# Kernel tuning notes

Measured on AMD Instinct MI355X. Metric: run time of the kernel, lower is better.

Reference implementation:

```python
import jax, jax.numpy as jnp
import numpy as np
import math

D_MODEL = 128      # embedding_dim
D_STATE = 64
D_CONV = 4
NHEADS = 4         # d_inner / headdim (Mamba2 default headdim=64)
HEADDIM = 64
D_INNER = 256      # expand * d_model
CONV_DIM = 384     # d_inner + 2*ngroups*d_state (ngroups=1)
D_IN_PROJ = 644    # 2*d_inner + 2*ngroups*d_state + nheads
NLAYERS = 2
INPUT_DIM = 768
EPS = 1e-5


def setup_inputs() -> dict:
    key = jax.random.key(0)
    ks = jax.random.split(key, 20)
    rn = lambda k, s, sd=0.02: jax.random.normal(k, s, jnp.float32) * sd
    return {
        "x": jax.random.normal(ks[0], (16, 1024, INPUT_DIM), jnp.float32),
        "fc1_W": rn(ks[1], (INPUT_DIM, D_MODEL)),
        "fc1_b": jnp.zeros((D_MODEL,), jnp.float32),
        "ln_w": jnp.ones((NLAYERS, D_MODEL), jnp.float32),
        "ln_b": jnp.zeros((NLAYERS, D_MODEL), jnp.float32),
        "in_W": rn(ks[2], (NLAYERS, D_MODEL, D_IN_PROJ)),
        "conv_w": rn(ks[3], (NLAYERS, D_CONV, CONV_DIM), 0.1),
        "conv_b": jnp.zeros((NLAYERS, CONV_DIM), jnp.float32),
        "dt_bias": rn(ks[4], (NLAYERS, NHEADS), 0.5),
        "A_log": jnp.log(jax.random.uniform(ks[5], (NLAYERS, NHEADS), jnp.float32, 1.0, 16.0)),
        "Dp": jnp.ones((NLAYERS, NHEADS), jnp.float32),
        "rms_w": jnp.ones((NLAYERS, D_INNER), jnp.float32),
        "out_W": rn(ks[6], (NLAYERS, D_INNER, D_MODEL)),
        "fc2_W1": rn(ks[7], (D_MODEL, D_MODEL)),
        "fc2_b1": jnp.zeros((D_MODEL,), jnp.float32),
        "fc2_W2": rn(ks[8], (D_MODEL, 6)),
        "fc2_b2": jnp.zeros((6,), jnp.float32),
    }


def _pos_embedding(L):
    pos = jnp.arange(L, dtype=jnp.float32)[:, None]                       # (L,1)
    div = jnp.exp(jnp.arange(0, D_MODEL, 2, dtype=jnp.float32) * (-math.log(10000.0) / D_MODEL))
    pe = jnp.zeros((L, D_MODEL), jnp.float32)
    pe = pe.at[:, 0::2].set(jnp.sin(pos * div))
    pe = pe.at[:, 1::2].set(jnp.cos(pos * div))
    return pe[None]                                                        # (1,L,D)


def _layernorm(x, w, b):
    mu = jnp.mean(x, -1, keepdims=True)
    var = jnp.mean(jnp.square(x - mu), -1, keepdims=True)
    return (x - mu) * jax.lax.rsqrt(var + EPS) * w + b


def _mamba2(u, in_W, conv_w, conv_b, dt_bias, A_log, Dp, rms_w, out_W):
    b, l, _ = u.shape
    zxbcdt = u @ in_W                                                      # (b,l,644)
    z = zxbcdt[..., :D_INNER]
    xBC = zxbcdt[..., D_INNER:D_INNER + CONV_DIM]
    dt = jax.nn.softplus(zxbcdt[..., D_INNER + CONV_DIM:] + dt_bias)       # (b,l,h)
    # causal depthwise conv1d (width 4) + SiLU
    xp = jnp.pad(xBC, ((0, 0), (D_CONV - 1, 0), (0, 0)))
    xc = conv_b
    for k in range(D_CONV):
        xc = xc + conv_w[k] * xp[:, k:k + l, :]
    xc = jax.nn.silu(xc)                                                   # (b,l,384)
    xh = xc[..., :D_INNER].reshape(b, l, NHEADS, HEADDIM)                  # (b,l,h,p)
    B = xc[..., D_INNER:D_INNER + D_STATE]                                 # (b,l,n)
    C = xc[..., D_INNER + D_STATE:]                                        # (b,l,n)
    A = -jnp.exp(A_log)                                                    # (h,)
    dA = jnp.exp(dt * A)                                                   # (b,l,h)
    dtx = dt[..., None] * xh                                               # (b,l,h,p)

    def step(h, inp):
        dA_t, dtx_t, B_t, C_t = inp                                        # (b,h),(b,h,p),(b,n),(b,n)
        h = dA_t[..., None, None] * h + dtx_t[..., None] * B_t[:, None, None, :]
        y = jnp.einsum('bhpn,bn->bhp', h, C_t)
        return h, y

    h0 = jnp.zeros((b, NHEADS, HEADDIM, D_STATE), u.dtype)
    _, ys = jax.lax.scan(step, h0, (dA.transpose(1, 0, 2), dtx.transpose(1, 0, 2, 3),
                                    B.transpose(1, 0, 2), C.transpose(1, 0, 2)))
    y = ys.transpose(1, 0, 2, 3) + Dp[None, None, :, None] * xh            # (b,l,h,p)
    y = y.reshape(b, l, D_INNER)
    # gated RMSNorm: rmsnorm(y * silu(z)) * weight
    y = y * jax.nn.silu(z)
    y = y * jax.lax.rsqrt(jnp.mean(jnp.square(y), -1, keepdims=True) + EPS) * rms_w
    return y @ out_W


def reference(x, fc1_W, fc1_b, ln_w, ln_b, in_W, conv_w, conv_b, dt_bias,
              A_log, Dp, rms_w, out_W, fc2_W1, fc2_b1, fc2_W2, fc2_b2):
    h = x @ fc1_W + fc1_b                                                  # (b,l,128)
    h = h + _pos_embedding(h.shape[1])
    for i in range(NLAYERS):
        res = h
        hn = _layernorm(h, ln_w[i], ln_b[i])
        h = _mamba2(hn, in_W[i], conv_w[i], conv_b[i], dt_bias[i],
                    A_log[i], Dp[i], rms_w[i], out_W[i]) + res
        # dropout: identity in eval mode
    h = jax.nn.leaky_relu(h @ fc2_W1 + fc2_b1, negative_slope=0.1)
    return h @ fc2_W2 + fc2_b2                                             # (b,l,6)
```

## Files before the change

### kernel.cpp

```cpp
#include <hip/hip_runtime.h>
#include <hip/hip_bf16.h>

#define BATCH 16
#define SEQ 1024
#define NROWS (BATCH*SEQ)
#define IN_DIM 768
#define DM 128
#define DIP 644
#define DI 256
#define CDIM 384
#define DST 64
#define NH 4
#define HD 64
#define CHUNK 64
#define NCHUNK (SEQ/CHUNK)

#define WB_FC1   0
#define WB_IN    98304
#define WB_OUT   263168
#define WB_FC2   328704
#define WB_TOTAL 345088

typedef __attribute__((ext_vector_type(8))) short short8;
typedef __attribute__((ext_vector_type(4))) float float4v;

__device__ __forceinline__ short f2b(float f) {
    unsigned u = __builtin_bit_cast(unsigned, f);
    u += 0x7fffu + ((u >> 16) & 1u);
    return (short)(u >> 16);
}
__device__ __forceinline__ float s2f(short s) {
    unsigned u = ((unsigned)(unsigned short)s) << 16;
    return __builtin_bit_cast(float, u);
}
__device__ __forceinline__ float silu(float a) { return a / (1.f + expf(-a)); }

__global__ void prep_weights(const float* __restrict__ fc1_W, const float* __restrict__ in_W,
                             const float* __restrict__ out_W, const float* __restrict__ fc2_W1,
                             short* __restrict__ wb) {
    int idx = blockIdx.x * 256 + threadIdx.x;
    if (idx < 98304) {
        int n = idx / 768, k = idx % 768;
        wb[WB_FC1 + idx] = f2b(fc1_W[k * 128 + n]);
        return;
    }
    idx -= 98304;
    if (idx < 2 * 82432) {
        int l = idx / 82432, r = idx % 82432;
        int n = r / 128, k = r % 128;
        wb[WB_IN + idx] = f2b(in_W[(size_t)l * 82432 + k * 644 + n]);
        return;
    }
    idx -= 164864;
    if (idx < 2 * 32768) {
        int l = idx / 32768, r = idx % 32768;
        int n = r / 256, k = r % 256;
        wb[WB_OUT + idx] = f2b(out_W[(size_t)l * 32768 + k * 128 + n]);
        return;
    }
    idx -= 65536;
    if (idx < 16384) {
        int n = idx / 128, k = idx % 128;
        wb[WB_FC2 + idx] = f2b(fc2_W1[k * 128 + n]);
    }
}

#define GEMM_PROLOGUE() \
    int tid = threadIdx.x; \
    int lane = tid & 63; \
    int m = lane & 15; \
    int kq = (lane >> 4) * 8; \
    int w = tid >> 6; \
    int mrow = (w & 3) * 16; \
    int ngrp = w >> 2; \
    int a_off = (mrow + m) * 72 + kq; \
    int b_off = (ngrp * 64 + m) * 72 + kq; \
    int ar = tid >> 3; \
    int ak = (tid & 7) * 8; \
    (void)ar; (void)ak; \
    float4v acc[4]; \
    acc[0] = (float4v)0.f; acc[1] = (float4v)0.f; acc[2] = (float4v)0.f; acc[3] = (float4v)0.f;

#define GEMM_COMPUTE_TILE() \
    { \
        short8 a0 = *reinterpret_cast<const short8*>(&As[a_off]); \
        short8 a1 = *reinterpret_cast<const short8*>(&As[a_off + 32]); \
        _Pragma("unroll") \
        for (int nt = 0; nt < 4; nt++) { \
            short8 b0 = *reinterpret_cast<const short8*>(&Bt[b_off + nt * 16 * 72]); \
            short8 b1 = *reinterpret_cast<const short8*>(&Bt[b_off + nt * 16 * 72 + 32]); \
            acc[nt] = __builtin_amdgcn_mfma_f32_16x16x32_bf16(a0, b0, acc[nt], 0, 0, 0); \
            acc[nt] = __builtin_amdgcn_mfma_f32_16x16x32_bf16(a1, b1, acc[nt], 0, 0, 0); \
        } \
    }

#define GEMM_STAGE_B(wtptr, LDB, k0) \
    _Pragma("unroll") \
    for (int i = 0; i < 2; i++) { \
        int idx = tid + i * 512; \
        int n = idx >> 3, kk = (idx & 7) * 8; \
        *reinterpret_cast<short8*>(&Bt[n * 72 + kk]) = \
            *reinterpret_cast<const short8*>(&wtptr[n * (LDB) + (k0) + kk]); \
    }

__global__ __launch_bounds__(512) void fc1_mfma(const float* __restrict__ x,
                                                const short* __restrict__ wt,
                                                const float* __restrict__ bias,
                                                const float* __restrict__ lnw0,
                                                const float* __restrict__ lnb0,
                                                float* __restrict__ h,
                                                short* __restrict__ hnb) {
    __shared__ short As[32 * 72];
    __shared__ short Bt[128 * 72];
    __shared__ float ps1[32][4], ps2[32][4];
    int tid = threadIdx.x;
    int lane = tid & 63;
    int m = lane & 15;
    int quad = lane >> 4;
    int kq = quad * 8;
    int w = tid >> 6;
    int mrow = (w & 1) * 16;
    int ngrp = w >> 1;
    int ar = tid >> 4;
    int ac = (tid & 15) * 4;
    int row0 = blockIdx.x * 32;
    float4v acc[2];
    acc[0] = (float4v)0.f; acc[1] = (float4v)0.f;
    for (int kt = 0; kt < 12; kt++) {
        int k0 = kt * 64;
        if (kt) __syncthreads();
        {
            const float* src = x + (size_t)(row0 + ar) * IN_DIM + k0 + ac;
            float4 v = *(const float4*)src;
            short4 pv;
            pv.x = f2b(v.x); pv.y = f2b(v.y); pv.z = f2b(v.z); pv.w = f2b(v.w);
            *reinterpret_cast<short4*>(&As[ar * 72 + ac]) = pv;
        }
        GEMM_STAGE_B(wt, 768, k0);
        __syncthreads();
        short8 a0 = *reinterpret_cast<const short8*>(&As[(mrow + m) * 72 + kq]);
        short8 a1 = *reinterpret_cast<const short8*>(&As[(mrow + m) * 72 + kq + 32]);
        #pragma unroll
        for (int nt = 0; nt < 2; nt++) {
            int bo = (ngrp * 32 + nt * 16 + m) * 72 + kq;
            short8 b0 = *reinterpret_cast<const short8*>(&Bt[bo]);
            short8 b1 = *reinterpret_cast<const short8*>(&Bt[bo + 32]);
            acc[nt] = __builtin_amdgcn_mfma_f32_16x16x32_bf16(a0, b0, acc[nt], 0, 0, 0);
            acc[nt] = __builtin_amdgcn_mfma_f32_16x16x32_bf16(a1, b1, acc[nt], 0, 0, 0);
        }
    }
    float val[2][4];
    float s1r[4] = {0.f,0.f,0.f,0.f}, s2r[4] = {0.f,0.f,0.f,0.f};
    #pragma unroll
    for (int nt = 0; nt < 2; nt++) {
        int col = ngrp * 32 + nt * 16 + m;
        float bv = bias[col];
        float div = expf(-(float)(col & ~1) * 0.071955784f);
        #pragma unroll
        for (int r = 0; r < 4; r++) {
            int row = row0 + mrow + quad * 4 + r;
            int t = row & (SEQ - 1);
            float arg = (float)t * div;
            float pe = (col & 1) ? cosf(arg) : sinf(arg);
            float v = acc[nt][r] + bv + pe;
            val[nt][r] = v;
            s1r[r] += v; s2r[r] += v * v;
        }
    }
    #pragma unroll
    for (int o = 1; o < 16; o <<= 1) {
        #pragma unroll
        for (int r = 0; r < 4; r++) {
            s1r[r] += __shfl_xor(s1r[r], o);
            s2r[r] += __shfl_xor(s2r[r], o);
        }
    }
    if (m == 0) {
        #pragma unroll
        for (int r = 0; r < 4; r++) {
            ps1[mrow + quad * 4 + r][ngrp] = s1r[r];
            ps2[mrow + quad * 4 + r][ngrp] = s2r[r];
        }
    }
    __syncthreads();
    #pragma unroll
    for (int r = 0; r < 4; r++) {
        int rl = mrow + quad * 4 + r;
        float s1 = ps1[rl][0] + ps1[rl][1] + ps1[rl][2] + ps1[rl][3];
        float s2 = ps2[rl][0] + ps2[rl][1] + ps2[rl][2] + ps2[rl][3];
        float mu = s1 * (1.f / 128.f);
        float rs = rsqrtf(s2 * (1.f / 128.f) - mu * mu + 1e-5f);
        int row = row0 + rl;
        #pragma unroll
        for (int nt = 0; nt < 2; nt++) {
            int col = ngrp * 32 + nt * 16 + m;
            float v = val[nt][r];
            h[(size_t)row * DM + col] = v;
            hnb[(size_t)row * DM + col] = f2b((v - mu) * rs * lnw0[col] + lnb0[col]);
        }
    }
}

__global__ __launch_bounds__(512) void inproj_mfma(const short* __restrict__ hnb,
                                                   const short* __restrict__ wb,
                                                   short* __restrict__ zb,
                                                   short* __restrict__ xbc,
                                                   int layer) {
    __shared__ short As[64 * 72];
    __shared__ short Bt[128 * 72];
    GEMM_PROLOGUE();
    int row0 = blockIdx.x * 64;
    int ncol0 = blockIdx.y * 128;
    const short* wt = wb + WB_IN + (size_t)layer * 82432;
    for (int kt = 0; kt < 2; kt++) {
        int k0 = kt * 64;
        if (kt) __syncthreads();
        *reinterpret_cast<short8*>(&As[ar * 72 + ak]) =
            *reinterpret_cast<const short8*>(&hnb[(size_t)(row0 + ar) * DM + k0 + ak]);
        #pragma unroll
        for (int i = 0; i < 2; i++) {
            int idx = tid + i * 512;
            int n = idx >> 3, kk = (idx & 7) * 8;
            *reinterpret_cast<short8*>(&Bt[n * 72 + kk]) =
                *reinterpret_cast<const short8*>(&wt[(ncol0 + n) * 128 + k0 + kk]);
        }
        __syncthreads();
        GEMM_COMPUTE_TILE();
    }
    int colbase = ncol0 + ngrp * 64;
    if (ncol0 < DI) {
        #pragma unroll
        for (int nt = 0; nt < 4; nt++) {
            int col = colbase + nt * 16 + m;
            #pragma unroll
            for (int r = 0; r < 4; r++) {
                int row = row0 + mrow + (lane >> 4) * 4 + r;
                zb[(size_t)row * DI + col] = f2b(acc[nt][r]);
            }
        }
    } else {
        int xbase = colbase - DI;
        #pragma unroll
        for (int nt = 0; nt < 4; nt++) {
            int col = xbase + nt * 16 + m;
            #pragma unroll
            for (int r = 0; r < 4; r++) {
                int row = row0 + mrow + (lane >> 4) * 4 + r;
                xbc[(size_t)row * CDIM + col] = f2b(acc[nt][r]);
            }
        }
    }
}

__global__ void conv_kernel(const short* __restrict__ xbc,
                            const float* __restrict__ convw, const float* __restrict__ convb,
                            short* __restrict__ xcb,
                            const short* __restrict__ hnb, const short* __restrict__ wb,
                            const float* __restrict__ dt_bias, float* __restrict__ dtb,
                            int layer) {
    int c = threadIdx.x;
    int row0 = blockIdx.x * 4;
    int l0 = row0 & (SEQ - 1);
    const float* cw = convw + (size_t)layer * 4 * CDIM;
    float w0 = cw[c], w1 = cw[CDIM + c], w2 = cw[2 * CDIM + c], w3 = cw[3 * CDIM + c];
    float bb = convb[layer * CDIM + c];
    float v[7];
    #pragma unroll
    for (int i = 0; i < 7; i++) {
        int rr = row0 + i - 3;
        v[i] = (l0 + i - 3 >= 0) ? s2f(xbc[(size_t)rr * CDIM + c]) : 0.f;
    }
    #pragma unroll
    for (int j = 0; j < 4; j++) {
        float acc = bb + w0 * v[j] + w1 * v[j + 1] + w2 * v[j + 2] + w3 * v[j + 3];
        xcb[(size_t)(row0 + j) * CDIM + c] = f2b(silu(acc));
    }
    if (c < 128) {
        int r = c >> 5;
        int rem = c & 31;
        int hh = rem >> 3;
        int part = rem & 7;
        const short* hrow = hnb + (size_t)(row0 + r) * DM + part * 16;
        const short* wrow = wb + WB_IN + (size_t)layer * 82432 + (640 + hh) * 128 + part * 16;
        short8 hv0 = *reinterpret_cast<const short8*>(hrow);
        short8 hv1 = *reinterpret_cast<const short8*>(hrow + 8);
        short8 wv0 = *reinterpret_cast<const short8*>(wrow);
        short8 wv1 = *reinterpret_cast<const short8*>(wrow + 8);
        float s = 0.f;
        #pragma unroll
        for (int q = 0; q < 8; q++)
            s += s2f(hv0[q]) * s2f(wv0[q]) + s2f(hv1[q]) * s2f(wv1[q]);
        s += __shfl_xor(s, 1);
        s += __shfl_xor(s, 2);
        s += __shfl_xor(s, 4);
        if (part == 0) {
            float raw = s + dt_bias[layer * NH + hh];
            float dt = (raw > 20.f) ? raw : log1pf(expf(raw));
            dtb[(size_t)(row0 + r) * NH + hh] = dt;
        }
    }
}

__global__ __launch_bounds__(256) void chunk_state_mfma(const short* __restrict__ xcb,
                                                        const float* __restrict__ dtb,
                                                        const float* __restrict__ A_log,
                                                        short* __restrict__ Slocb,
                                                        float* __restrict__ decay, int layer) {
    __shared__ short XTw[64 * 72];
    __shared__ short BT[64 * 72];
    __shared__ float wst[64];
    int bid = blockIdx.x;
    int c  = bid & (NCHUNK - 1);
    int hh = (bid >> 4) & (NH - 1);
    int b  = bid >> 6;
    int tid = threadIdx.x;
    int row0 = b * SEQ + c * CHUNK;
    float A = -expf(A_log[layer * NH + hh]);

    if (tid < CHUNK) {
        float dtv = dtb[(size_t)(row0 + tid) * NH + hh];
        float l = dtv * A;
        #pragma unroll
        for (int o = 1; o < 64; o <<= 1) { float v = __shfl_up(l, o); if (tid >= o) l += v; }
        float Ltot = __shfl(l, 63);
        wst[tid] = expf(Ltot - l) * dtv;
        if (tid == 63) decay[bid] = expf(Ltot);
    }
    __syncthreads();
    {
        int p = tid & 63;
        int tb0 = tid >> 6;
        #pragma unroll
        for (int i = 0; i < 2; i++) {
            int t0 = (tb0 + i * 4) * 8;
            short8 xv, bv;
            #pragma unroll
            for (int j = 0; j < 8; j++) {
                int t = t0 + j;
                const short* xr = xcb + (size_t)(row0 + t) * CDIM;
                xv[j] = f2b(s2f(xr[hh * HD + p]) * wst[t]);
                bv[j] = xr[DI + p];
            }
            *reinterpret_cast<short8*>(&XTw[p * 72 + t0]) = xv;
            *reinterpret_cast<short8*>(&BT[p * 72 + t0]) = bv;
        }
    }
    __syncthreads();

    int lane = tid & 63;
    int m = lane & 15;
    int kq = (lane >> 4) * 8;
    int w = tid >> 6;
    int a_off = (w * 16 + m) * 72 + kq;
    float4v acc[4];
    acc[0] = (float4v)0.f; acc[1] = (float4v)0.f; acc[2] = (float4v)0.f; acc[3] = (float4v)0.f;
    short8 a0 = *reinterpret_cast<const short8*>(&XTw[a_off]);
    short8 a1 = *reinterpret_cast<const short8*>(&XTw[a_off + 32]);
    #pragma unroll
    for (int nt = 0; nt < 4; nt++) {
        int bo = (nt * 16 + m) * 72 + kq;
        short8 b0 = *reinterpret_cast<const short8*>(&BT[bo]);
        short8 b1 = *reinterpret_cast<const short8*>(&BT[bo + 32]);
        acc[nt] = __builtin_amdgcn_mfma_f32_16x16x32_bf16(a0, b0, acc[nt], 0, 0, 0);
        acc[nt] = __builtin_amdgcn_mfma_f32_16x16x32_bf16(a1, b1, acc[nt], 0, 0, 0);
    }
    short* Sp = Slocb + (size_t)bid * (HD * DST);
    int tq = (lane >> 4) * 4;
    #pragma unroll
    for (int nt = 0; nt < 4; nt++) {
        #pragma unroll
        for (int r = 0; r < 4; r++) {
            int p = w * 16 + tq + r;
            int n = nt * 16 + m;
            Sp[p * DST + n] = f2b(acc[nt][r]);
        }
    }
}

__global__ __launch_bounds__(256) void chunk_out_mfma(const short* __restrict__ xcb,
                                                      const float* __restrict__ dtb,
                                                      const float* __restrict__ A_log,
                                                      const float* __restrict__ Dpw,
                                                      const short* __restrict__ Slocb,
                                                      const float* __restrict__ decay,
                                                      short* __restrict__ ybb, int layer) {
    __shared__ short Cb[64 * 72];
    __shared__ short Bb[64 * 72];
    __shared__ short XT[64 * 72];
    __shared__ short HT[64 * 72];
    __shared__ float Ls[64], dts[64];
    int bid = blockIdx.x;
    int c  = bid & (NCHUNK - 1);
    int hh = (bid >> 4) & (NH - 1);
    int b  = bid >> 6;
    int tid = threadIdx.x;
    int row0 = b * SEQ + c * CHUNK;
    int bh0 = bid & ~(NCHUNK - 1);
    float A = -expf(A_log[layer * NH + hh]);
    float Dph = Dpw[layer * NH + hh];

    if (tid < CHUNK) {
        float dtv = dtb[(size_t)(row0 + tid) * NH + hh];
        float l = dtv * A;
        #pragma unroll
        for (int o = 1; o < 64; o <<= 1) { float v = __shfl_up(l, o); if (tid >= o) l += v; }
        Ls[tid] = l;
        dts[tid] = dtv;
    }
    {
        float hreg[16];
        #pragma unroll
        for (int k = 0; k < 16; k++) hreg[k] = 0.f;
        for (int j = 0; j < c; j++) {
            float d = decay[bh0 + j];
            const short* Sp = Slocb + (size_t)(bh0 + j) * (HD * DST) + tid * 16;
            short8 s0 = *reinterpret_cast<const short8*>(Sp);
            short8 s1 = *reinterpret_cast<const short8*>(Sp + 8);
            #pragma unroll
            for (int k = 0; k < 8; k++) {
                hreg[k]     = d * hreg[k]     + s2f(s0[k]);
                hreg[8 + k] = d * hreg[8 + k] + s2f(s1[k]);
            }
        }
        int p = tid >> 2;
        int n0 = (tid & 3) * 16;
        short8 h0, h1;
        #pragma unroll
        for (int k = 0; k < 8; k++) { h0[k] = f2b(hreg[k]); h1[k] = f2b(hreg[8 + k]); }
        *reinterpret_cast<short8*>(&HT[p * 72 + n0]) = h0;
        *reinterpret_cast<short8*>(&HT[p * 72 + n0 + 8]) = h1;
    }
    {
        int p = tid & 63;
        int tb0 = tid >> 6;
        #pragma unroll
        for (int i = 0; i < 2; i++) {
            int t0 = (tb0 + i * 4) * 8;
            short8 xv;
            #pragma unroll
            for (int j = 0; j < 8; j++)
                xv[j] = xcb[(size_t)(row0 + t0 + j) * CDIM + hh * HD + p];
            *reinterpret_cast<short8*>(&XT[p * 72 + t0]) = xv;
        }
    }
    #pragma unroll
    for (int i = 0; i < 2; i++) {
        int idx = tid + i * 256;
        int t = idx >> 3, cb = (idx & 7) * 8;
        const short* xr = xcb + (size_t)(row0 + t) * CDIM;
        *reinterpret_cast<short8*>(&Bb[t * 72 + cb]) =
            *reinterpret_cast<const short8*>(&xr[DI + cb]);
        *reinterpret_cast<short8*>(&Cb[t * 72 + cb]) =
            *reinterpret_cast<const short8*>(&xr[DI + DST + cb]);
    }
    __syncthreads();

    int lane = tid & 63;
    int m = lane & 15;
    int kq = (lane >> 4) * 8;
    int w = tid >> 6;
    int tq = (lane >> 4) * 4;
    int a_off = (w * 16 + m) * 72 + kq;

    short8 ca0 = *reinterpret_cast<const short8*>(&Cb[a_off]);
    short8 ca1 = *reinterpret_cast<const short8*>(&Cb[a_off + 32]);

    float4v g[4], ir[4];
    #pragma unroll
    for (int i = 0; i < 4; i++) { g[i] = (float4v)0.f; ir[i] = (float4v)0.f; }
    #pragma unroll
    for (int st = 0; st < 4; st++) {
        int bo = (st * 16 + m) * 72 + kq;
        short8 b0 = *reinterpret_cast<const short8*>(&Bb[bo]);
        short8 b1 = *reinterpret_cast<const short8*>(&Bb[bo + 32]);
        g[st] = __builtin_amdgcn_mfma_f32_16x16x32_bf16(ca0, b0, g[st], 0, 0, 0);
        g[st] = __builtin_amdgcn_mfma_f32_16x16x32_bf16(ca1, b1, g[st], 0, 0, 0);
        short8 h0 = *reinterpret_cast<const short8*>(&HT[bo]);
        short8 h1 = *reinterpret_cast<const short8*>(&HT[bo + 32]);
        ir[st] = __builtin_amdgcn_mfma_f32_16x16x32_bf16(ca0, h0, ir[st], 0, 0, 0);
        ir[st] = __builtin_amdgcn_mfma_f32_16x16x32_bf16(ca1, h1, ir[st], 0, 0, 0);
    }
    __syncthreads();
    #pragma unroll
    for (int st = 0; st < 4; st++) {
        #pragma unroll
        for (int r = 0; r < 4; r++) {
            int t = w * 16 + tq + r;
            int s = st * 16 + m;
            float mv = 0.f;
            if (s <= t) mv = g[st][r] * expf(Ls[t] - Ls[s]) * dts[s];
            Bb[t * 72 + s] = f2b(mv);
        }
    }
    __syncthreads();
    float4v yi[4];
    #pragma unroll
    for (int i = 0; i < 4; i++) yi[i] = (float4v)0.f;
    short8 ma0 = *reinterpret_cast<const short8*>(&Bb[a_off]);
    short8 ma1 = *reinterpret_cast<const short8*>(&Bb[a_off + 32]);
    #pragma unroll
    for (int pt = 0; pt < 4; pt++) {
        int bo = (pt * 16 + m) * 72 + kq;
        short8 x0 = *reinterpret_cast<const short8*>(&XT[bo]);
        short8 x1 = *reinterpret_cast<const short8*>(&XT[bo + 32]);
        yi[pt] = __builtin_amdgcn_mfma_f32_16x16x32_bf16(ma0, x0, yi[pt], 0, 0, 0);
        yi[pt] = __builtin_amdgcn_mfma_f32_16x16x32_bf16(ma1, x1, yi[pt], 0, 0, 0);
    }
    #pragma unroll
    for (int r = 0; r < 4; r++) {
        int t = w * 16 + tq + r;
        float et = expf(Ls[t]);
        short* yr = ybb + (size_t)(row0 + t) * DI + hh * HD;
        #pragma unroll
        for (int pt = 0; pt < 4; pt++) {
            int p = pt * 16 + m;
            float xv = s2f(XT[p * 72 + t]);
            yr[p] = f2b(yi[pt][r] + et * ir[pt][r] + Dph * xv);
        }
    }
}

__global__ __launch_bounds__(512) void outproj_gate_mfma(const short* __restrict__ ybb,
                                                         const short* __restrict__ zb,
                                                         const float* __restrict__ rmsw,
                                                         const short* __restrict__ wb,
                                                         const float* __restrict__ lnw2,
                                                         const float* __restrict__ lnb2,
                                                         float* __restrict__ h,
                                                         short* __restrict__ hnb,
                                                         const float* __restrict__ fc2_b1,
                                                         const float* __restrict__ fc2_W2,
                                                         const float* __restrict__ fc2_b2,
                                                         float* __restrict__ outp,
                                                         int layer, int do_fc2) {
    __shared__ __align__(16) char smem[36864];
    short* As = (short*)smem;
    short* Bt = (short*)(smem + 9216);
    float* hs = (float*)smem;
    short* As2 = (short*)smem;
    short* Bt2 = (short*)(smem + 17408);
    float* h2s = (float*)smem;
    __shared__ float rs_s[64];
    __shared__ float w2s[768];
    GEMM_PROLOGUE();
    int row0 = blockIdx.x * 64;
    const short* wt = wb + WB_OUT + (size_t)layer * 32768;
    if (do_fc2)
        for (int i = tid; i < 768; i += 512) w2s[i] = fc2_W2[i];
    {
        int r = tid >> 3, j = tid & 7;
        const short8* yr = (const short8*)(ybb + (size_t)(row0 + r) * DI + j * 32);
        const short8* zr = (const short8*)(zb + (size_t)(row0 + r) * DI + j * 32);
        float s2 = 0.f;
        #pragma unroll
        for (int i = 0; i < 4; i++) {
            short8 yv = yr[i];
            short8 zv = zr[i];
            #pragma unroll
            for (int q = 0; q < 8; q++) {
                float v = s2f(yv[q]) * silu(s2f(zv[q]));
                s2 += v * v;
            }
        }
        #pragma unroll
        for (int o = 1; o < 8; o <<= 1) s2 += __shfl_xor(s2, o);
        if (j == 0) rs_s[r] = rsqrtf(s2 * (1.f / 256.f) + 1e-5f);
    }
    __syncthreads();
    for (int kt = 0; kt < 4; kt++) {
        int k0 = kt * 64;
        if (kt) __syncthreads();
        {
            int k = k0 + ak;
            short8 yv = *(const short8*)(ybb + (size_t)(row0 + ar) * DI + k);
            short8 zv = *(const short8*)(zb + (size_t)(row0 + ar) * DI + k);
            float4 w0 = *(const float4*)(rmsw + layer * DI + k);
            float4 w1 = *(const float4*)(rmsw + layer * DI + k + 4);
            float rs = rs_s[ar];
            short8 av;
            av[0] = f2b(s2f(yv[0]) * silu(s2f(zv[0])) * rs * w0.x);
            av[1] = f2b(s2f(yv[1]) * silu(s2f(zv[1])) * rs * w0.y);
            av[2] = f2b(s2f(yv[2]) * silu(s2f(zv[2])) * rs * w0.z);
            av[3] = f2b(s2f(yv[3]) * silu(s2f(zv[3])) * rs * w0.w);
            av[4] = f2b(s2f(yv[4]) * silu(s2f(zv[4])) * rs * w1.x);
            av[5] = f2b(s2f(yv[5]) * silu(s2f(zv[5])) * rs * w1.y);
            av[6] = f2b(s2f(yv[6]) * silu(s2f(zv[6])) * rs * w1.z);
            av[7] = f2b(s2f(yv[7]) * silu(s2f(zv[7])) * rs * w1.w);
            *reinterpret_cast<short8*>(&As[ar * 72 + ak]) = av;
        }
        GEMM_STAGE_B(wt, 256, k0);
        __syncthreads();
        GEMM_COMPUTE_TILE();
    }
    __syncthreads();
    #pragma unroll
    for (int nt = 0; nt < 4; nt++) {
        int col = ngrp * 64 + nt * 16 + m;
        #pragma unroll
        for (int r = 0; r < 4; r++) {
            int rr = mrow + (lane >> 4) * 4 + r;
            hs[rr * 133 + col] = acc[nt][r];
        }
    }
    __syncthreads();
    int er = tid >> 3, ej = tid & 7;
    int erow = row0 + er;
    float vals[16];
    {
        const float* hsrc = h + (size_t)erow * DM + ej * 16;
        float s1 = 0.f, s2 = 0.f;
        #pragma unroll
        for (int i = 0; i < 4; i++) {
            float4 ho = *(const float4*)(hsrc + i * 4);
            float v0 = ho.x + hs[er * 133 + ej * 16 + i * 4];
            float v1 = ho.y + hs[er * 133 + ej * 16 + i * 4 + 1];
            float v2 = ho.z + hs[er * 133 + ej * 16 + i * 4 + 2];
            float v3 = ho.w + hs[er * 133 + ej * 16 + i * 4 + 3];
            vals[i*4] = v0; vals[i*4+1] = v1; vals[i*4+2] = v2; vals[i*4+3] = v3;
            s1 += v0 + v1 + v2 + v3;
            s2 += v0*v0 + v1*v1 + v2*v2 + v3*v3;
        }
        if (!do_fc2) {
            #pragma unroll
            for (int o = 1; o < 8; o <<= 1) { s1 += __shfl_xor(s1, o); s2 += __shfl_xor(s2, o); }
            float* hdst = h + (size_t)erow * DM + ej * 16;
            #pragma unroll
            for (int i = 0; i < 4; i++)
                *(float4*)(hdst + i * 4) = make_float4(vals[i*4], vals[i*4+1], vals[i*4+2], vals[i*4+3]);
            float mu = s1 * (1.f / 128.f);
            float rs = rsqrtf(s2 * (1.f / 128.f) - mu * mu + 1e-5f);
            const float* lw = lnw2 + ej * 16;
            const float* lb = lnb2 + ej * 16;
            short8 a0, a1;
            #pragma unroll
            for (int i = 0; i < 8; i++) {
                a0[i] = f2b((vals[i] - mu) * rs * lw[i] + lb[i]);
                a1[i] = f2b((vals[8 + i] - mu) * rs * lw[8 + i] + lb[8 + i]);
            }
            short* hndst = hnb + (size_t)erow * DM + ej * 16;
            *reinterpret_cast<short8*>(hndst) = a0;
            *reinterpret_cast<short8*>(hndst + 8) = a1;
        }
    }
    if (!do_fc2) return;

    __syncthreads();
    {
        short8 a0p, a1p;
        #pragma unroll
        for (int i = 0; i < 8; i++) { a0p[i] = f2b(vals[i]); a1p[i] = f2b(vals[8 + i]); }
        *reinterpret_cast<short8*>(&As2[er * 136 + ej * 16]) = a0p;
        *reinterpret_cast<short8*>(&As2[er * 136 + ej * 16 + 8]) = a1p;
    }
    const short* wtf = wb + WB_FC2;
    float4v acc2[4];
    acc2[0] = (float4v)0.f; acc2[1] = (float4v)0.f; acc2[2] = (float4v)0.f; acc2[3] = (float4v)0.f;
    for (int kt = 0; kt < 2; kt++) {
        int k0 = kt * 64;
        __syncthreads();
        #pragma unroll
        for (int i = 0; i < 2; i++) {
            int idx = tid + i * 512;
            int n = idx >> 3, kk = (idx & 7) * 8;
            *reinterpret_cast<short8*>(&Bt2[n * 72 + kk]) =
                *reinterpret_cast<const short8*>(&wtf[n * 128 + k0 + kk]);
        }
        __syncthreads();
        short8 a0 = *reinterpret_cast<const short8*>(&As2[(mrow + m) * 136 + k0 + kq]);
        short8 a1 = *reinterpret_cast<const short8*>(&As2[(mrow + m) * 136 + k0 + kq + 32]);
        #pragma unroll
        for (int nt = 0; nt < 4; nt++) {
            int bo = (ngrp * 64 + nt * 16 + m) * 72 + kq;
            short8 b0 = *reinterpret_cast<const short8*>(&Bt2[bo]);
            short8 b1 = *reinterpret_cast<const short8*>(&Bt2[bo + 32]);
            acc2[nt] = __builtin_amdgcn_mfma_f32_16x16x32_bf16(a0, b0, acc2[nt], 0, 0, 0);
            acc2[nt] = __builtin_amdgcn_mfma_f32_16x16x32_bf16(a1, b1, acc2[nt], 0, 0, 0);
        }
    }
    __syncthreads();
    #pragma unroll
    for (int nt = 0; nt < 4; nt++) {
        int col = ngrp * 64 + nt * 16 + m;
        float bv = fc2_b1[col];
        #pragma unroll
        for (int r = 0; r < 4; r++) {
            int rr = mrow + (lane >> 4) * 4 + r;
            float o = acc2[nt][r] + bv;
            h2s[rr * 132 + col] = (o > 0.f) ? o : 0.1f * o;
        }
    }
    __syncthreads();
    if (tid < 384) {
        int r = tid / 6, cc = tid % 6;
        float a2 = fc2_b2[cc];
        #pragma unroll 16
        for (int k = 0; k < 128; k++) a2 += h2s[r * 132 + k] * w2s[k * 6 + cc];
        outp[(size_t)(row0 + r) * 6 + cc] = a2;
    }
}

extern "C" void kernel_launch(void* const* d_in, const int* in_sizes, int n_in,
                              void* d_out, int out_size, void* d_ws, size_t ws_size,
                              hipStream_t stream) {
    const float* x       = (const float*)d_in[0];
    const float* fc1_W   = (const float*)d_in[1];
    const float* fc1_b   = (const float*)d_in[2];
    const float* ln_w    = (const float*)d_in[3];
    const float* ln_b    = (const float*)d_in[4];
    const float* in_W    = (const float*)d_in[5];
    const float* conv_w  = (const float*)d_in[6];
    const float* conv_b  = (const float*)d_in[7];
    const float* dt_bias = (const float*)d_in[8];
    const float* A_log   = (const float*)d_in[9];
    const float* Dp      = (const float*)d_in[10];
    const float* rms_w   = (const float*)d_in[11];
    const float* out_W   = (const float*)d_in[12];
    const float* fc2_W1  = (const float*)d_in[13];
    const float* fc2_b1  = (const float*)d_in[14];
    const float* fc2_W2  = (const float*)d_in[15];
    const float* fc2_b2  = (const float*)d_in[16];
    float* out = (float*)d_out;

    float* ws = (float*)d_ws;
    float* h     = ws;
    float* dtb   = h     + (size_t)NROWS * DM;
    float* decay = dtb   + (size_t)NROWS * NH;
    short* sbase = (short*)(decay + 1024);
    short* hnb   = sbase;
    short* zb    = hnb   + (size_t)NROWS * DM;
    short* xbc   = zb    + (size_t)NROWS * DI;
    short* xcb   = xbc   + (size_t)NROWS * CDIM;
    short* ybb   = xcb   + (size_t)NROWS * CDIM;
    short* Slocb = ybb   + (size_t)NROWS * DI;
    short* wb    = Slocb + (size_t)BATCH*NH*NCHUNK*HD*DST;

    prep_weights<<<1348, 256, 0, stream>>>(fc1_W, in_W, out_W, fc2_W1, wb);
    fc1_mfma<<<NROWS / 32, 512, 0, stream>>>(x, wb + WB_FC1, fc1_b, ln_w, ln_b, h, hnb);

    for (int layer = 0; layer < 2; layer++) {
        inproj_mfma<<<dim3(NROWS / 64, 5), 512, 0, stream>>>(hnb, wb, zb, xbc, layer);
        conv_kernel<<<NROWS / 4, CDIM, 0, stream>>>(xbc, conv_w, conv_b, xcb,
                                                    hnb, wb, dt_bias, dtb, layer);
        chunk_state_mfma<<<BATCH*NH*NCHUNK, 256, 0, stream>>>(xcb, dtb, A_log, Slocb, decay, layer);
        chunk_out_mfma<<<BATCH*NH*NCHUNK, 256, 0, stream>>>(xcb, dtb, A_log, Dp, Slocb, decay,
                                                            ybb, layer);
        outproj_gate_mfma<<<NROWS / 64, 512, 0, stream>>>(ybb, zb, rms_w, wb,
                                                          ln_w + DM, ln_b + DM, h, hnb,
                                                          fc2_b1, fc2_W2, fc2_b2, out,
                                                          layer, layer == 1 ? 1 : 0);
    }
}
```

Baseline: 257.2 us.

## Double-buffer fc1 and outproj weight tiles and shrink outproj row tile

fc1 now double-buffers its A/B shared-memory tiles, so the next k-tile is staged while MFMAs run on the current one, which removes one barrier per iteration. outproj_gate is restructured to 32-row blocks: it computes the gated RMSNorm once into a full-width A tile held in shared memory, double-buffers the out_W tiles, loads the whole fc2_W1 at once, and splits the final 6-column dot product across two threads. Twice as many blocks run, which should improve occupancy and cut repeated y/z reads and extra barriers. The cost is more shared memory per block, and each block now re-stages the weights for half as many rows.

```diff
diff --git a/kernel.cpp b/kernel.cpp
--- a/kernel.cpp
+++ b/kernel.cpp
@@ -94,15 +94,6 @@
         } \
     }
 
-#define GEMM_STAGE_B(wtptr, LDB, k0) \
-    _Pragma("unroll") \
-    for (int i = 0; i < 2; i++) { \
-        int idx = tid + i * 512; \
-        int n = idx >> 3, kk = (idx & 7) * 8; \
-        *reinterpret_cast<short8*>(&Bt[n * 72 + kk]) = \
-            *reinterpret_cast<const short8*>(&wtptr[n * (LDB) + (k0) + kk]); \
-    }
-
 __global__ __launch_bounds__(512) void fc1_mfma(const float* __restrict__ x,
                                                 const short* __restrict__ wt,
                                                 const float* __restrict__ bias,
@@ -110,8 +101,8 @@
                                                 const float* __restrict__ lnb0,
                                                 float* __restrict__ h,
                                                 short* __restrict__ hnb) {
-    __shared__ short As[32 * 72];
-    __shared__ short Bt[128 * 72];
+    __shared__ short As[2][32 * 72];
+    __shared__ short Bt[2][128 * 72];
     __shared__ float ps1[32][4], ps2[32][4];
     int tid = threadIdx.x;
     int lane = tid & 63;
@@ -126,28 +117,38 @@
     int row0 = blockIdx.x * 32;
     float4v acc[2];
     acc[0] = (float4v)0.f; acc[1] = (float4v)0.f;
+
+#define FC1_STAGE(BI, KT) { \
+        const float* src = x + (size_t)(row0 + ar) * IN_DIM + (KT) * 64 + ac; \
+        float4 v = *(const float4*)src; \
+        short4 pv; pv.x = f2b(v.x); pv.y = f2b(v.y); pv.z = f2b(v.z); pv.w = f2b(v.w); \
+        *reinterpret_cast<short4*>(&As[BI][ar * 72 + ac]) = pv; \
+        _Pragma("unroll") \
+        for (int i = 0; i < 2; i++) { \
+            int idx = tid + i * 512; \
+            int n = idx >> 3, kk = (idx & 7) * 8; \
+            *reinterpret_cast<short8*>(&Bt[BI][n * 72 + kk]) = \
+                *reinterpret_cast<const short8*>(&wt[n * 768 + (KT) * 64 + kk]); \
+        } }
+
+    FC1_STAGE(0, 0)
+    __syncthreads();
+    int buf = 0;
     for (int kt = 0; kt < 12; kt++) {
-        int k0 = kt * 64;
-        if (kt) __syncthreads();
-        {
-            const float* src = x + (size_t)(row0 + ar) * IN_DIM + k0 + ac;
-            float4 v = *(const float4*)src;
-            short4 pv;
-            pv.x = f2b(v.x); pv.y = f2b(v.y); pv.z = f2b(v.z); pv.w = f2b(v.w);
-            *reinterpret_cast<short4*>(&As[ar * 72 + ac]) = pv;
-        }
-        GEMM_STAGE_B(wt, 768, k0);
-        __syncthreads();
-        short8 a0 = *reinterpret_cast<const short8*>(&As[(mrow + m) * 72 + kq]);
-        short8 a1 = *reinterpret_cast<const short8*>(&As[(mrow + m) * 72 + kq + 32]);
+        int nb = buf ^ 1;
+        if (kt < 11) FC1_STAGE(nb, kt + 1)
+        short8 a0 = *reinterpret_cast<const short8*>(&As[buf][(mrow + m) * 72 + kq]);
+        short8 a1 = *reinterpret_cast<const short8*>(&As[buf][(mrow + m) * 72 + kq + 32]);
         #pragma unroll
         for (int nt = 0; nt < 2; nt++) {
             int bo = (ngrp * 32 + nt * 16 + m) * 72 + kq;
-            short8 b0 = *reinterpret_cast<const short8*>(&Bt[bo]);
-            short8 b1 = *reinterpret_cast<const short8*>(&Bt[bo + 32]);
+            short8 b0 = *reinterpret_cast<const short8*>(&Bt[buf][bo]);
+            short8 b1 = *reinterpret_cast<const short8*>(&Bt[buf][bo + 32]);
             acc[nt] = __builtin_amdgcn_mfma_f32_16x16x32_bf16(a0, b0, acc[nt], 0, 0, 0);
             acc[nt] = __builtin_amdgcn_mfma_f32_16x16x32_bf16(a1, b1, acc[nt], 0, 0, 0);
         }
+        __syncthreads();
+        buf = nb;
     }
     float val[2][4];
     float s1r[4] = {0.f,0.f,0.f,0.f}, s2r[4] = {0.f,0.f,0.f,0.f};
@@ -533,144 +534,151 @@
                                                          const float* __restrict__ fc2_b2,
                                                          float* __restrict__ outp,
                                                          int layer, int do_fc2) {
-    __shared__ __align__(16) char smem[36864];
-    short* As = (short*)smem;
-    short* Bt = (short*)(smem + 9216);
-    float* hs = (float*)smem;
-    short* As2 = (short*)smem;
-    short* Bt2 = (short*)(smem + 17408);
-    float* h2s = (float*)smem;
-    __shared__ float rs_s[64];
+    __shared__ __align__(16) short As[32 * 264];
+    __shared__ __align__(16) short Bt[2][128 * 72];
     __shared__ float w2s[768];
-    GEMM_PROLOGUE();
-    int row0 = blockIdx.x * 64;
+    int tid = threadIdx.x;
+    int lane = tid & 63;
+    int m = lane & 15;
+    int quad = lane >> 4;
+    int kq = quad * 8;
+    int w = tid >> 6;
+    int mrow = (w & 1) * 16;
+    int ngrp = w >> 1;
+    int row0 = blockIdx.x * 32;
     const short* wt = wb + WB_OUT + (size_t)layer * 32768;
     if (do_fc2)
         for (int i = tid; i < 768; i += 512) w2s[i] = fc2_W2[i];
     {
-        int r = tid >> 3, j = tid & 7;
-        const short8* yr = (const short8*)(ybb + (size_t)(row0 + r) * DI + j * 32);
-        const short8* zr = (const short8*)(zb + (size_t)(row0 + r) * DI + j * 32);
-        float s2 = 0.f;
-        #pragma unroll
-        for (int i = 0; i < 4; i++) {
-            short8 yv = yr[i];
-            short8 zv = zr[i];
-            #pragma unroll
-            for (int q = 0; q < 8; q++) {
-                float v = s2f(yv[q]) * silu(s2f(zv[q]));
-                s2 += v * v;
-            }
-        }
-        #pragma unroll
-        for (int o = 1; o < 8; o <<= 1) s2 += __shfl_xor(s2, o);
-        if (j == 0) rs_s[r] = rsqrtf(s2 * (1.f / 256.f) + 1e-5f);
-    }
-    __syncthreads();
+        int r = tid >> 4, j = tid & 15;
+        const short* yr = ybb + (size_t)(row0 + r) * DI + j * 16;
+        const short* zr = zb + (size_t)(row0 + r) * DI + j * 16;
+        short8 y0 = *reinterpret_cast<const short8*>(yr);
+        short8 y1 = *reinterpret_cast<const short8*>(yr + 8);
+        short8 z0 = *reinterpret_cast<const short8*>(zr);
+        short8 z1 = *reinterpret_cast<const short8*>(zr + 8);
+        float v[16]; float s2 = 0.f;
+        #pragma unroll
+        for (int q = 0; q < 8; q++) {
+            v[q]     = s2f(y0[q]) * silu(s2f(z0[q]));
+            v[8 + q] = s2f(y1[q]) * silu(s2f(z1[q]));
+        }
+        #pragma unroll
+        for (int q = 0; q < 16; q++) s2 += v[q] * v[q];
+        #pragma unroll
+        for (int o = 1; o < 16; o <<= 1) s2 += __shfl_xor(s2, o);
+        float rs = rsqrtf(s2 * (1.f / 256.f) + 1e-5f);
+        const float* rw = rmsw + layer * DI + j * 16;
+        short8 a0, a1;
+        #pragma unroll
+        for (int q = 0; q < 8; q++) {
+            a0[q] = f2b(v[q] * rs * rw[q]);
+            a1[q] = f2b(v[8 + q] * rs * rw[8 + q]);
+        }
+        *reinterpret_cast<short8*>(&As[r * 264 + j * 16]) = a0;
+        *reinterpret_cast<short8*>(&As[r * 264 + j * 16 + 8]) = a1;
+    }
+    {
+        int n = tid >> 2, kk = (tid & 3) * 16;
+        *reinterpret_cast<short8*>(&Bt[0][n * 72 + kk]) =
+            *reinterpret_cast<const short8*>(&wt[n * 256 + kk]);
+        *reinterpret_cast<short8*>(&Bt[0][n * 72 + kk + 8]) =
+            *reinterpret_cast<const short8*>(&wt[n * 256 + kk + 8]);
+    }
+    __syncthreads();
+    float4v acc[2];
+    acc[0] = (float4v)0.f; acc[1] = (float4v)0.f;
+    int buf = 0;
     for (int kt = 0; kt < 4; kt++) {
-        int k0 = kt * 64;
-        if (kt) __syncthreads();
-        {
-            int k = k0 + ak;
-            short8 yv = *(const short8*)(ybb + (size_t)(row0 + ar) * DI + k);
-            short8 zv = *(const short8*)(zb + (size_t)(row0 + ar) * DI + k);
-            float4 w0 = *(const float4*)(rmsw + layer * DI + k);
-            float4 w1 = *(const float4*)(rmsw + layer * DI + k + 4);
-            float rs = rs_s[ar];
-            short8 av;
-            av[0] = f2b(s2f(yv[0]) * silu(s2f(zv[0])) * rs * w0.x);
-            av[1] = f2b(s2f(yv[1]) * silu(s2f(zv[1])) * rs * w0.y);
-            av[2] = f2b(s2f(yv[2]) * silu(s2f(zv[2])) * rs * w0.z);
-            av[3] = f2b(s2f(yv[3]) * silu(s2f(zv[3])) * rs * w0.w);
-            av[4] = f2b(s2f(yv[4]) * silu(s2f(zv[4])) * rs * w1.x);
-            av[5] = f2b(s2f(yv[5]) * silu(s2f(zv[5])) * rs * w1.y);
-            av[6] = f2b(s2f(yv[6]) * silu(s2f(zv[6])) * rs * w1.z);
-            av[7] = f2b(s2f(yv[7]) * silu(s2f(zv[7])) * rs * w1.w);
-            *reinterpret_cast<short8*>(&As[ar * 72 + ak]) = av;
-        }
-        GEMM_STAGE_B(wt, 256, k0);
+        if (kt < 3) {
+            int n = tid >> 2, kk = (tid & 3) * 16;
+            *reinterpret_cast<short8*>(&Bt[buf ^ 1][n * 72 + kk]) =
+                *reinterpret_cast<const short8*>(&wt[n * 256 + (kt + 1) * 64 + kk]);
+            *reinterpret_cast<short8*>(&Bt[buf ^ 1][n * 72 + kk + 8]) =
+                *reinterpret_cast<const short8*>(&wt[n * 256 + (kt + 1) * 64 + kk + 8]);
+        }
+        short8 a0 = *reinterpret_cast<const short8*>(&As[(mrow + m) * 264 + kt * 64 + kq]);
+        short8 a1 = *reinterpret_cast<const short8*>(&As[(mrow + m) * 264 + kt * 64 + kq + 32]);
+        #pragma unroll
+        for (int nt = 0; nt < 2; nt++) {
+            int bo = (ngrp * 32 + nt * 16 + m) * 72 + kq;
+            short8 b0 = *reinterpret_cast<const short8*>(&Bt[buf][bo]);
+            short8 b1 = *reinterpret_cast<const short8*>(&Bt[buf][bo + 32]);
+            acc[nt] = __builtin_amdgcn_mfma_f32_16x16x32_bf16(a0, b0, acc[nt], 0, 0, 0);
+            acc[nt] = __builtin_amdgcn_mfma_f32_16x16x32_bf16(a1, b1, acc[nt], 0, 0, 0);
+        }
         __syncthreads();
-        GEMM_COMPUTE_TILE();
-    }
-    __syncthreads();
-    #pragma unroll
-    for (int nt = 0; nt < 4; nt++) {
-        int col = ngrp * 64 + nt * 16 + m;
-        #pragma unroll
-        for (int r = 0; r < 4; r++) {
-            int rr = mrow + (lane >> 4) * 4 + r;
-            hs[rr * 133 + col] = acc[nt][r];
-        }
-    }
-    __syncthreads();
-    int er = tid >> 3, ej = tid & 7;
+        buf ^= 1;
+    }
+    float* hs = (float*)As;
+    #pragma unroll
+    for (int nt = 0; nt < 2; nt++) {
+        int col = ngrp * 32 + nt * 16 + m;
+        #pragma unroll
+        for (int r = 0; r < 4; r++)
+            hs[(mrow + quad * 4 + r) * 132 + col] = acc[nt][r];
+    }
+    __syncthreads();
+    int er = tid >> 4, ej = tid & 15;
     int erow = row0 + er;
-    float vals[16];
+    float vals[8];
+    float s1 = 0.f, s2v = 0.f;
     {
-        const float* hsrc = h + (size_t)erow * DM + ej * 16;
-        float s1 = 0.f, s2 = 0.f;
-        #pragma unroll
-        for (int i = 0; i < 4; i++) {
-            float4 ho = *(const float4*)(hsrc + i * 4);
-            float v0 = ho.x + hs[er * 133 + ej * 16 + i * 4];
-            float v1 = ho.y + hs[er * 133 + ej * 16 + i * 4 + 1];
-            float v2 = ho.z + hs[er * 133 + ej * 16 + i * 4 + 2];
-            float v3 = ho.w + hs[er * 133 + ej * 16 + i * 4 + 3];
-            vals[i*4] = v0; vals[i*4+1] = v1; vals[i*4+2] = v2; vals[i*4+3] = v3;
-            s1 += v0 + v1 + v2 + v3;
-            s2 += v0*v0 + v1*v1 + v2*v2 + v3*v3;
-        }
-        if (!do_fc2) {
-            #pragma unroll
-            for (int o = 1; o < 8; o <<= 1) { s1 += __shfl_xor(s1, o); s2 += __shfl_xor(s2, o); }
-            float* hdst = h + (size_t)erow * DM + ej * 16;
-            #pragma unroll
-            for (int i = 0; i < 4; i++)
-                *(float4*)(hdst + i * 4) = make_float4(vals[i*4], vals[i*4+1], vals[i*4+2], vals[i*4+3]);
-            float mu = s1 * (1.f / 128.f);
-            float rs = rsqrtf(s2 * (1.f / 128.f) - mu * mu + 1e-5f);
-            const float* lw = lnw2 + ej * 16;
-            const float* lb = lnb2 + ej * 16;
-            short8 a0, a1;
-            #pragma unroll
-            for (int i = 0; i < 8; i++) {
-                a0[i] = f2b((vals[i] - mu) * rs * lw[i] + lb[i]);
-                a1[i] = f2b((vals[8 + i] - mu) * rs * lw[8 + i] + lb[8 + i]);
-            }
-            short* hndst = hnb + (size_t)erow * DM + ej * 16;
-            *reinterpret_cast<short8*>(hndst) = a0;
-            *reinterpret_cast<short8*>(hndst + 8) = a1;
-        }
-    }
-    if (!do_fc2) return;
-
-    __syncthreads();
+        const float* hsrc = h + (size_t)erow * DM + ej * 8;
+        float4 h0 = *(const float4*)hsrc;
+        float4 h1 = *(const float4*)(hsrc + 4);
+        const float* hrow = &hs[er * 132 + ej * 8];
+        float4 q0 = *(const float4*)hrow;
+        float4 q1 = *(const float4*)(hrow + 4);
+        vals[0] = h0.x + q0.x; vals[1] = h0.y + q0.y; vals[2] = h0.z + q0.z; vals[3] = h0.w + q0.w;
+        vals[4] = h1.x + q1.x; vals[5] = h1.y + q1.y; vals[6] = h1.z + q1.z; vals[7] = h1.w + q1.w;
+        #pragma unroll
+        for (int i = 0; i < 8; i++) { s1 += vals[i]; s2v += vals[i] * vals[i]; }
+    }
+    if (!do_fc2) {
+        #pragma unroll
+        for (int o = 1; o < 16; o <<= 1) { s1 += __shfl_xor(s1, o); s2v += __shfl_xor(s2v, o); }
+        float* hdst = h + (size_t)erow * DM + ej * 8;
+        *(float4*)hdst = make_float4(vals[0], vals[1], vals[2], vals[3]);
+        *(float4*)(hdst + 4) = make_float4(vals[4], vals[5], vals[6], vals[7]);
+        float mu = s1 * (1.f / 128.f);
+        float rs2 = rsqrtf(s2v * (1.f / 128.f) - mu * mu + 1e-5f);
+        const float* lw = lnw2 + ej * 8;
+        const float* lb = lnb2 + ej * 8;
+        short8 a0;
+        #pragma unroll
+        for (int i = 0; i < 8; i++) a0[i] = f2b((vals[i] - mu) * rs2 * lw[i] + lb[i]);
+        *reinterpret_cast<short8*>(hnb + (size_t)erow * DM + ej * 8) = a0;
+        return;
+    }
+    __syncthreads();
+    short* As2 = (short*)As;
     {
-        short8 a0p, a1p;
-        #pragma unroll
-        for (int i = 0; i < 8; i++) { a0p[i] = f2b(vals[i]); a1p[i] = f2b(vals[8 + i]); }
-        *reinterpret_cast<short8*>(&As2[er * 136 + ej * 16]) = a0p;
-        *reinterpret_cast<short8*>(&As2[er * 136 + ej * 16 + 8]) = a1p;
+        short8 ap;
+        #pragma unroll
+        for (int i = 0; i < 8; i++) ap[i] = f2b(vals[i]);
+        *reinterpret_cast<short8*>(&As2[er * 136 + ej * 8]) = ap;
     }
     const short* wtf = wb + WB_FC2;
-    float4v acc2[4];
-    acc2[0] = (float4v)0.f; acc2[1] = (float4v)0.f; acc2[2] = (float4v)0.f; acc2[3] = (float4v)0.f;
+    short* Bt2 = (short*)Bt;
+    {
+        int n = tid >> 2, kk = (tid & 3) * 32;
+        #pragma unroll
+        for (int i = 0; i < 4; i++)
+            *reinterpret_cast<short8*>(&Bt2[n * 136 + kk + i * 8]) =
+                *reinterpret_cast<const short8*>(&wtf[n * 128 + kk + i * 8]);
+    }
+    __syncthreads();
+    float4v acc2[2];
+    acc2[0] = (float4v)0.f; acc2[1] = (float4v)0.f;
+    #pragma unroll
     for (int kt = 0; kt < 2; kt++) {
         int k0 = kt * 64;
-        __syncthreads();
-        #pragma unroll
-        for (int i = 0; i < 2; i++) {
-            int idx = tid + i * 512;
-            int n = idx >> 3, kk = (idx & 7) * 8;
-            *reinterpret_cast<short8*>(&Bt2[n * 72 + kk]) =
-                *reinterpret_cast<const short8*>(&wtf[n * 128 + k0 + kk]);
-        }
-        __syncthreads();
         short8 a0 = *reinterpret_cast<const short8*>(&As2[(mrow + m) * 136 + k0 + kq]);
         short8 a1 = *reinterpret_cast<const short8*>(&As2[(mrow + m) * 136 + k0 + kq + 32]);
         #pragma unroll
-        for (int nt = 0; nt < 4; nt++) {
-            int bo = (ngrp * 64 + nt * 16 + m) * 72 + kq;
+        for (int nt = 0; nt < 2; nt++) {
+            int bo = (ngrp * 32 + nt * 16 + m) * 136 + k0 + kq;
             short8 b0 = *reinterpret_cast<const short8*>(&Bt2[bo]);
             short8 b1 = *reinterpret_cast<const short8*>(&Bt2[bo + 32]);
             acc2[nt] = __builtin_amdgcn_mfma_f32_16x16x32_bf16(a0, b0, acc2[nt], 0, 0, 0);
@@ -678,24 +686,26 @@
         }
     }
     __syncthreads();
-    #pragma unroll
-    for (int nt = 0; nt < 4; nt++) {
-        int col = ngrp * 64 + nt * 16 + m;
+    float* h2s = (float*)As;
+    #pragma unroll
+    for (int nt = 0; nt < 2; nt++) {
+        int col = ngrp * 32 + nt * 16 + m;
         float bv = fc2_b1[col];
         #pragma unroll
         for (int r = 0; r < 4; r++) {
-            int rr = mrow + (lane >> 4) * 4 + r;
             float o = acc2[nt][r] + bv;
-            h2s[rr * 132 + col] = (o > 0.f) ? o : 0.1f * o;
+            h2s[(mrow + quad * 4 + r) * 132 + col] = (o > 0.f) ? o : 0.1f * o;
         }
     }
     __syncthreads();
     if (tid < 384) {
-        int r = tid / 6, cc = tid % 6;
-        float a2 = fc2_b2[cc];
-        #pragma unroll 16
-        for (int k = 0; k < 128; k++) a2 += h2s[r * 132 + k] * w2s[k * 6 + cc];
-        outp[(size_t)(row0 + r) * 6 + cc] = a2;
+        int r = tid / 12, q = tid % 12, cc = q >> 1, part = q & 1;
+        float a2 = 0.f;
+        #pragma unroll 8
+        for (int k = 0; k < 64; k++)
+            a2 += h2s[r * 132 + part * 64 + k] * w2s[(part * 64 + k) * 6 + cc];
+        a2 += __shfl_xor(a2, 1);
+        if (!part) outp[(size_t)(row0 + r) * 6 + cc] = fc2_b2[cc] + a2;
     }
 }
 
@@ -744,7 +754,7 @@
         chunk_state_mfma<<<BATCH*NH*NCHUNK, 256, 0, stream>>>(xcb, dtb, A_log, Slocb, decay, layer);
         chunk_out_mfma<<<BATCH*NH*NCHUNK, 256, 0, stream>>>(xcb, dtb, A_log, Dp, Slocb, decay,
                                                             ybb, layer);
-        outproj_gate_mfma<<<NROWS / 64, 512, 0, stream>>>(ybb, zb, rms_w, wb,
+        outproj_gate_mfma<<<NROWS / 32, 512, 0, stream>>>(ybb, zb, rms_w, wb,
                                                           ln_w + DM, ln_b + DM, h, hnb,
                                                           fc2_b1, fc2_W2, fc2_b2, out,
                                                           layer, layer == 1 ? 1 : 0);
```

Result: faster. 247.1 us (-3.9%).
